# Kernel tuning notes

Hardware: AMD Instinct MI355X
Metric: run time of the kernel (lower is better)

The kernel has to match this reference:

```python
import jax, jax.numpy as jnp
import numpy as np

EPS = 1e-12

def l2norm(x):
    # matches torch F.normalize(dim=-1): x / max(||x||, eps)
    n = jnp.sqrt(jnp.sum(x * x, axis=-1, keepdims=True))
    return x / jnp.maximum(n, EPS)

def setup_inputs() -> dict:
    key = jax.random.key(0)
    ks = jax.random.split(key, 5)
    B, N, D, W = 128, 196, 768, 32
    image_features = jax.random.normal(ks[0], (B, D), jnp.float32)
    text_features = jax.random.normal(ks[1], (B, D), jnp.float32)
    image_token_features = jax.random.normal(ks[2], (B, N, D), jnp.float32)
    concept_text_features = jax.random.normal(ks[3], (B, W, D), jnp.float32)
    concept_counts = jax.random.randint(ks[4], (B,), 1, W + 1, dtype=jnp.int32)
    logit_scale = jnp.asarray(np.log(10.0), jnp.float32)   # SigLIP-style init
    logit_bias = jnp.asarray(-10.0, jnp.float32)
    return dict(image_features=image_features, text_features=text_features,
                image_token_features=image_token_features,
                concept_text_features=concept_text_features,
                concept_counts=concept_counts,
                logit_scale=logit_scale, logit_bias=logit_bias)

def _sigmoid_contrastive(logits):
    B = logits.shape[0]
    logits = jnp.clip(logits, -50.0, 50.0)
    z = 2.0 * jnp.eye(B, dtype=logits.dtype) - 1.0  # +1 diag, -1 off-diag
    return -jnp.mean(jax.nn.log_sigmoid(z * logits))

def reference(image_features, text_features, image_token_features,
              concept_text_features, concept_counts, logit_scale, logit_bias,
              alpha=0.5):
    t = jnp.exp(jnp.clip(logit_scale, -10.0, 10.0))

    # ---- IT-Align (SigLIP sigmoid contrastive on CLS features) ----
    img = l2norm(image_features)          # (B, D)
    txt = l2norm(text_features)           # (B, D)
    it_logits = t * (img @ txt.T) + logit_bias
    it_loss = _sigmoid_contrastive(it_logits)

    # ---- RC-Align (region-concept max-pool alignment, dense/masked) ----
    patches = l2norm(image_token_features)        # (B, N, D)
    concepts = l2norm(concept_text_features)      # (B, W, D)
    W = concepts.shape[1]
    # A[m, v, n, w] = cos(patch n of image m, concept w of sample v)
    A = jnp.einsum('mnd,vwd->mvnw', patches, concepts)
    max_per_concept = jnp.max(A, axis=2)          # (B, B, W) max over patches
    mask = (jnp.arange(W)[None, :] < concept_counts[:, None]).astype(patches.dtype)  # (B, W)
    counts = concept_counts.astype(patches.dtype)  # (B,)
    # S[m, v] = mean over valid concepts of sample v of max-pooled sims
    S = jnp.sum(max_per_concept * mask[None, :, :], axis=-1) / counts[None, :]
    rc_logits = t * S + logit_bias
    rc_loss = _sigmoid_contrastive(rc_logits)

    total = it_loss + alpha * rc_loss
    return total, it_loss, rc_loss
```

## Files before the change

kernel.cpp:

```cpp
#include <hip/hip_runtime.h>
#include <hip/hip_bf16.h>
#include <cstdint>

using i32x4 = __attribute__((ext_vector_type(4))) int;

#define BATCH   128
#define NPATCH  196
#define MTOT    25088
#define MT      98
#define DDIM    768
#define WCON    32
#define NCOLS   4096
#define BNC     128
#define NBN     32
#define NT      12
#define NBLK    3136

#define PB_PAT  0
#define NPAT2   (MTOT/2)
#define PB_CON  (NPAT2)
#define NCON2   (NCOLS/2)
#define PB_IMG  (PB_CON + NCON2)
#define PB_TXT  (PB_IMG + BATCH)
#define PB_MAX  (PB_TXT + BATCH)
#define PB_CIDX (PB_MAX + 64)
#define PB_N    (PB_CIDX + 1)

#define PI8_OFF   0ull
#define PI8_BYTES ((size_t)MTOT*DDIM)
#define CI8_OFF   (PI8_OFF + PI8_BYTES)
#define CI8_BYTES (4096ull*DDIM)
#define SP_OFF    (CI8_OFF + CI8_BYTES)
#define SP_BYTES  ((size_t)MTOT*4)
#define SC_OFF    (SP_OFF + SP_BYTES)
#define SC_BYTES  (4096ull*4)
#define IMGN_OFF  (SC_OFF + SC_BYTES)
#define F_BYTES   (128ull*768*4)
#define TXTN_OFF  (IMGN_OFF + F_BYTES)
#define MAX_OFF   (TXTN_OFF + F_BYTES)
#define MAX_BYTES (128ull*4096*4)
#define PART_OFF  (MAX_OFF + MAX_BYTES)
#define CIDX_OFF  (PART_OFF + 1024ull)
#define NCC_OFF   (CIDX_OFF + 4096ull*4)
#define WS_NEED   (NCC_OFF + 256ull)

__device__ __forceinline__ void async_cp16(void* lds_p, const void* g) {
  __builtin_amdgcn_global_load_lds(
      (const __attribute__((address_space(1))) unsigned int*)g,
      (__attribute__((address_space(3))) unsigned int*)lds_p, 16, 0, 0);
}

__device__ __forceinline__ float neg_log_sigmoid(float x) {
  return (x > 0.f) ? log1pf(expf(-x)) : (log1pf(expf(x)) - x);
}

__device__ __forceinline__ int encf(float f) {
  int i = __float_as_int(f);
  return i >= 0 ? i : (i ^ 0x7FFFFFFF);
}
__device__ __forceinline__ float decf(int e) {
  return __int_as_float(e >= 0 ? e : (e ^ 0x7FFFFFFF));
}

template<int VM>
__device__ __forceinline__ void vmwait() {
  asm volatile("s_waitcnt vmcnt(%0)" :: "n"(VM) : "memory");
}
__device__ __forceinline__ void blockbar() {
  asm volatile("" ::: "memory");
  __builtin_amdgcn_s_barrier();
  asm volatile("" ::: "memory");
}

__global__ void preproc_kernel(const float* __restrict__ tokp, char* __restrict__ outp,
                               float* __restrict__ srowp,
                               const float* __restrict__ tokc, char* __restrict__ outc,
                               float* __restrict__ srowc,
                               const float* __restrict__ imgf, float* __restrict__ imgn,
                               const float* __restrict__ txtf, float* __restrict__ txtn,
                               const int* __restrict__ counts,
                               int* __restrict__ Maxbuf,
                               int* __restrict__ cidx, int* __restrict__ ncc) {
  int bid = blockIdx.x;
  int t = threadIdx.x;

  if (bid >= PB_MAX) {
    if (bid < PB_CIDX) {
      int r = bid - PB_MAX;
      int4* dst = (int4*)(Maxbuf + (size_t)r * 8192);
      int4 pat = make_int4(0x80808080, 0x80808080, 0x80808080, 0x80808080);
      #pragma unroll
      for (int i = 0; i < 11; ++i) {
        int idx = t + i*192;
        if (idx < 2048) dst[idx] = pat;
      }
    } else {
      __shared__ int cls[128];
      __shared__ int stot;
      if (t < 128) cls[t] = counts[t];
      __syncthreads();
      if (t < 128) {
        int base = 0;
        for (int i = 0; i < t; ++i) base += cls[i];
        int cnt = cls[t];
        for (int k = 0; k < cnt; ++k) cidx[base + k] = t * 32 + k;
        if (t == 127) stot = base + cnt;
      }
      __syncthreads();
      if (t == 0) {
        int tot = stot;
        int totp = (tot + 127) & ~127;
        for (int j = tot; j < totp; ++j) cidx[j] = -1;
        ncc[0] = totp;
      }
    }
    return;
  }

  if (bid >= PB_IMG) {
    const float* in;
    float* fout;
    if (bid < PB_TXT) {
      int r = bid - PB_IMG;
      in = imgf + (size_t)r * DDIM; fout = imgn + (size_t)r * DDIM;
    } else {
      int r = bid - PB_TXT;
      in = txtf + (size_t)r * DDIM; fout = txtn + (size_t)r * DDIM;
    }
    __shared__ float sbs[3];
    float4 v = ((const float4*)in)[t];
    float ss = v.x*v.x + v.y*v.y + v.z*v.z + v.w*v.w;
    #pragma unroll
    for (int o = 32; o; o >>= 1) ss += __shfl_down(ss, o);
    if ((t & 63) == 0) sbs[t >> 6] = ss;
    __syncthreads();
    float tot = sbs[0] + sbs[1] + sbs[2];
    float scale = 1.0f / fmaxf(sqrtf(tot), 1e-12f);
    ((float4*)fout)[t] = make_float4(v.x*scale, v.y*scale, v.z*scale, v.w*scale);
    return;
  }

  const float *inA, *inB;
  char *qoutA, *qoutB;
  float *srowA, *srowB;
  bool validA = true, validB = true;
  if (bid < PB_CON) {
    int r = bid * 2;
    inA = tokp + (size_t)r * DDIM;       inB = inA + DDIM;
    qoutA = outp + (size_t)r * DDIM;     qoutB = qoutA + DDIM;
    srowA = srowp + r;                   srowB = srowA + 1;
  } else {
    int r = (bid - PB_CON) * 2;
    int cnt = counts[r >> 5];
    validA = (r & 31) < cnt;
    validB = ((r & 31) + 1) < cnt;
    if (!validA && !validB) return;
    inA = tokc + (size_t)r * DDIM;       inB = inA + DDIM;
    qoutA = outc + (size_t)r * DDIM;     qoutB = qoutA + DDIM;
    srowA = srowc + r;                   srowB = srowA + 1;
  }

  __shared__ float sA[3], aA[3], sB[3], aB[3];
  float4 vA = validA ? ((const float4*)inA)[t] : make_float4(0,0,0,0);
  float4 vB = validB ? ((const float4*)inB)[t] : make_float4(0,0,0,0);
  float ssA = vA.x*vA.x + vA.y*vA.y + vA.z*vA.z + vA.w*vA.w;
  float ssB = vB.x*vB.x + vB.y*vB.y + vB.z*vB.z + vB.w*vB.w;
  float amA = fmaxf(fmaxf(fabsf(vA.x), fabsf(vA.y)), fmaxf(fabsf(vA.z), fabsf(vA.w)));
  float amB = fmaxf(fmaxf(fabsf(vB.x), fabsf(vB.y)), fmaxf(fabsf(vB.z), fabsf(vB.w)));
  #pragma unroll
  for (int o = 32; o; o >>= 1) {
    ssA += __shfl_down(ssA, o);  amA = fmaxf(amA, __shfl_down(amA, o));
    ssB += __shfl_down(ssB, o);  amB = fmaxf(amB, __shfl_down(amB, o));
  }
  if ((t & 63) == 0) {
    sA[t >> 6] = ssA; aA[t >> 6] = amA;
    sB[t >> 6] = ssB; aB[t >> 6] = amB;
  }
  __syncthreads();
  float totA = sA[0] + sA[1] + sA[2];
  float totB = sB[0] + sB[1] + sB[2];
  float amxA = fmaxf(fmaxf(aA[0], aA[1]), fmaxf(aA[2], 1e-30f));
  float amxB = fmaxf(fmaxf(aB[0], aB[1]), fmaxf(aB[2], 1e-30f));

  if (validA) {
    float qs = 127.0f / amxA;
    int qx = (int)rintf(vA.x * qs), qy = (int)rintf(vA.y * qs);
    int qz = (int)rintf(vA.z * qs), qw = (int)rintf(vA.w * qs);
    ((uint*)qoutA)[t] = (uint)(qx & 0xff) | ((uint)(qy & 0xff) << 8) |
                        ((uint)(qz & 0xff) << 16) | ((uint)(qw & 0xff) << 24);
    if (t == 0) srowA[0] = amxA / (127.0f * fmaxf(sqrtf(totA), 1e-12f));
  }
  if (validB) {
    float qs = 127.0f / amxB;
    int qx = (int)rintf(vB.x * qs), qy = (int)rintf(vB.y * qs);
    int qz = (int)rintf(vB.z * qs), qw = (int)rintf(vB.w * qs);
    ((uint*)qoutB)[t] = (uint)(qx & 0xff) | ((uint)(qy & 0xff) << 8) |
                        ((uint)(qz & 0xff) << 16) | ((uint)(qw & 0xff) << 24);
    if (t == 0) srowB[0] = amxB / (127.0f * fmaxf(sqrtf(totB), 1e-12f));
  }
}

__global__ __launch_bounds__(256, 2)
void rc_gemm_max_kernel(const char* __restrict__ patches,
                        const char* __restrict__ concepts,
                        const float* __restrict__ sp,
                        const float* __restrict__ sc,
                        const int* __restrict__ cidx,
                        const int* __restrict__ ncc,
                        int* __restrict__ Max) {
  __shared__ __align__(16) char lds[3 * 24576];
  __shared__ float sp_lds[256];
  __shared__ float colmax[2][2][128];

  const int bid0 = blockIdx.x;
  const int lin = (bid0 & 7) * 392 + (bid0 >> 3);
  const int mt = lin >> 5;
  const int bn = lin & 31;
  const int bcol = bn * BNC;
  const int totp = __builtin_amdgcn_readfirstlane(ncc[0]);
  if (bcol >= totp) return;

  const int tid = threadIdx.x;
  const int lane = tid & 63;
  const int wid = tid >> 6;
  const int wm = wid >> 1;
  const int wn = wid & 1;
  const int brow = mt * 256;

  const char* Ab = patches + (size_t)brow * DDIM;

  sp_lds[tid] = sp[brow + tid];

  const int arow = wm*128 + (lane & 15);
  const int aslot = (lane >> 4) ^ (((lane & 15) >> 1) & 3);
  const int a_base = arow*64 + aslot*16;
  const int bcl = wn*64 + (lane & 15);
  const int b_base = 16384 + bcl*64 + aslot*16;
  const int r0 = tid >> 2;
  const int q0 = (tid & 3) ^ ((r0 >> 1) & 3);
  const int svoff = r0*DDIM + q0*16;

  const int cr0 = cidx[bcol + (tid >> 2)];
  const int cr1 = cidx[bcol + 64 + (tid >> 2)];
  const char* bp0 = concepts + (size_t)(cr0 < 0 ? 0 : cr0) * DDIM + q0*16;
  const char* bp1 = concepts + (size_t)(cr1 < 0 ? 0 : cr1) * DDIM + q0*16;

  i32x4 acc[8][4];
  #pragma unroll
  for (int i = 0; i < 8; ++i)
    #pragma unroll
    for (int j = 0; j < 4; ++j) { i32x4 z = {0,0,0,0}; acc[i][j] = z; }

  auto stage = [&](int t, int bufi) {
    char* dst = lds + bufi * 24576;
    const int kcol = t * 64;
    #pragma unroll
    for (int k2 = 0; k2 < 4; ++k2)
      async_cp16(dst + tid*16 + k2*4096, Ab + svoff + k2*(64*DDIM) + kcol);
    async_cp16(dst + 16384 + tid*16,        bp0 + kcol);
    async_cp16(dst + 16384 + tid*16 + 4096, bp1 + kcol);
  };

  auto compute = [&](int bufi) {
    const char* ab = lds + bufi * 24576;
    i32x4 a[8], b[4];
    #pragma unroll
    for (int i = 0; i < 8; ++i) a[i] = *(const i32x4*)(ab + a_base + i*1024);
    #pragma unroll
    for (int j = 0; j < 4; ++j) b[j] = *(const i32x4*)(ab + b_base + j*1024);
    __builtin_amdgcn_s_setprio(1);
    #pragma unroll
    for (int i = 0; i < 8; ++i)
      #pragma unroll
      for (int j = 0; j < 4; ++j)
        acc[i][j] = __builtin_amdgcn_mfma_i32_16x16x64_i8(a[i], b[j], acc[i][j], 0, 0, 0);
    __builtin_amdgcn_s_setprio(0);
  };

#define TILE(T, VMN, DOSTAGE)                                                 \
  {                                                                           \
    if (DOSTAGE) stage((T) + 2, ((T) + 2) % 3);                               \
    vmwait<VMN>();                                                            \
    blockbar();                                                               \
    compute((T) % 3);                                                         \
    blockbar();                                                               \
  }

  stage(0, 0);
  stage(1, 1);
  TILE(0, 12, 1)  TILE(1, 12, 1)  TILE(2, 12, 1)  TILE(3, 12, 1)
  TILE(4, 12, 1)  TILE(5, 12, 1)  TILE(6, 12, 1)  TILE(7, 12, 1)
  TILE(8, 12, 1)  TILE(9, 12, 1)  TILE(10, 6, 0)  TILE(11, 0, 0)
#undef TILE

  float cmax[4][2];
  #pragma unroll
  for (int j = 0; j < 4; ++j) { cmax[j][0] = -3e38f; cmax[j][1] = -3e38f; }
  float scv[4];
  #pragma unroll
  for (int j = 0; j < 4; ++j) {
    int oc = cidx[bcol + wn*64 + j*16 + (lane & 15)];
    scv[j] = sc[oc < 0 ? 0 : oc];
  }
  const int img0w = (brow + wm*128) / NPATCH;
  #pragma unroll
  for (int i = 0; i < 8; ++i) {
    #pragma unroll
    for (int e = 0; e < 4; ++e) {
      int rl = wm*128 + i*16 + (lane >> 4)*4 + e;
      float spv = sp_lds[rl];
      int seg = ((brow + rl) / NPATCH) - img0w;
      #pragma unroll
      for (int j = 0; j < 4; ++j) {
        float v = (float)acc[i][j][e] * spv * scv[j];
        cmax[j][0] = (seg == 0) ? fmaxf(cmax[j][0], v) : cmax[j][0];
        cmax[j][1] = (seg == 1) ? fmaxf(cmax[j][1], v) : cmax[j][1];
      }
    }
  }
  #pragma unroll
  for (int j = 0; j < 4; ++j) {
    #pragma unroll
    for (int s = 0; s < 2; ++s) {
      float v = cmax[j][s];
      v = fmaxf(v, __shfl_xor(v, 16));
      v = fmaxf(v, __shfl_xor(v, 32));
      cmax[j][s] = v;
    }
  }
  if (lane < 16) {
    #pragma unroll
    for (int j = 0; j < 4; ++j) {
      colmax[wm][0][wn*64 + j*16 + lane] = cmax[j][0];
      colmax[wm][1][wn*64 + j*16 + lane] = cmax[j][1];
    }
  }
  __syncthreads();
  {
    int w = tid >> 7;
    int col = tid & 127;
    int oc = cidx[bcol + col];
    if (oc >= 0) {
      int i0 = (brow + w*128) / NPATCH;
      int i1 = (brow + w*128 + 127) / NPATCH;
      atomicMax(&Max[(size_t)i0 * NCOLS + oc], encf(colmax[w][0][col]));
      if (i1 != i0) atomicMax(&Max[(size_t)i1 * NCOLS + oc], encf(colmax[w][1][col]));
    }
  }
}

__global__ void loss_kernel(const float* __restrict__ imgn, const float* __restrict__ txtn,
                            const int* __restrict__ Max, const int* __restrict__ counts,
                            const float* __restrict__ sc, const float* __restrict__ bi,
                            float* __restrict__ part) {
  int bid = blockIdx.x;
  int c = threadIdx.x;
  float t = expf(fminf(fmaxf(sc[0], -10.f), 10.f));
  float val;
  int m;
  if (bid < BATCH) {
    m = bid;
    __shared__ __align__(16) float arow[DDIM];
    for (int k = c; k < DDIM; k += 128) arow[k] = imgn[(size_t)m * DDIM + k];
    __syncthreads();
    const float4* br = (const float4*)(txtn + (size_t)c * DDIM);
    const float4* ar = (const float4*)arow;
    float dot = 0.f;
    #pragma unroll 8
    for (int k = 0; k < DDIM/4; ++k) {
      float4 x = ar[k], y = br[k];
      dot += x.x*y.x + x.y*y.y + x.z*y.z + x.w*y.w;
    }
    float logit = fminf(fmaxf(t*dot + bi[0], -50.f), 50.f);
    val = neg_log_sigmoid((c == m) ? logit : -logit);
  } else {
    m = bid - BATCH;
    const int* row = Max + (size_t)m * NCOLS + (size_t)c * WCON;
    int cnt = counts[c];
    float s = 0.f;
    for (int w = 0; w < cnt; ++w) s += decf(row[w]);
    float S = s / (float)cnt;
    float logit = fminf(fmaxf(t*S + bi[0], -50.f), 50.f);
    val = neg_log_sigmoid((c == m) ? logit : -logit);
  }
  __shared__ float sb[2];
  #pragma unroll
  for (int o = 32; o; o >>= 1) val += __shfl_down(val, o);
  if ((c & 63) == 0) sb[c >> 6] = val;
  __syncthreads();
  if (c == 0) part[bid] = sb[0] + sb[1];
}

__global__ void finalize_kernel(const float* __restrict__ part, float* __restrict__ out) {
  int t = threadIdx.x;
  float v = part[t];
  __shared__ float sb[4];
  #pragma unroll
  for (int o = 32; o; o >>= 1) v += __shfl_down(v, o);
  if ((t & 63) == 0) sb[t >> 6] = v;
  __syncthreads();
  if (t == 0) {
    float it = (sb[0] + sb[1]) * (1.f / 16384.f);
    float rc = (sb[2] + sb[3]) * (1.f / 16384.f);
    out[0] = it + 0.5f * rc;
    out[1] = it;
    out[2] = rc;
  }
}


extern "C" void kernel_launch(void* const* d_in, const int* in_sizes, int n_in,
                              void* d_out, int out_size, void* d_ws, size_t ws_size,
                              hipStream_t stream) {
  const float* image_features        = (const float*)d_in[0];
  const float* text_features         = (const float*)d_in[1];
  const float* image_token_features  = (const float*)d_in[2];
  const float* concept_text_features = (const float*)d_in[3];
  const int*   concept_counts        = (const int*)d_in[4];
  const float* logit_scale           = (const float*)d_in[5];
  const float* logit_bias            = (const float*)d_in[6];
  float* out = (float*)d_out;

  if (ws_size < WS_NEED) {
    hipMemsetAsync(d_out, 0, (size_t)out_size * sizeof(float), stream);
    return;
  }

  char* ws = (char*)d_ws;
  char*  patches_i8  = ws + PI8_OFF;
  char*  concepts_i8 = ws + CI8_OFF;
  float* sp          = (float*)(ws + SP_OFF);
  float* scq         = (float*)(ws + SC_OFF);
  float* imgn        = (float*)(ws + IMGN_OFF);
  float* txtn        = (float*)(ws + TXTN_OFF);
  int*   Maxbuf      = (int*)(ws + MAX_OFF);
  float* part        = (float*)(ws + PART_OFF);
  int*   cidx        = (int*)(ws + CIDX_OFF);
  int*   ncc         = (int*)(ws + NCC_OFF);

  preproc_kernel<<<PB_N, 192, 0, stream>>>(
      image_token_features, patches_i8, sp,
      concept_text_features, concepts_i8, scq,
      image_features, imgn, text_features, txtn,
      concept_counts, Maxbuf, cidx, ncc);

  rc_gemm_max_kernel<<<NBLK, 256, 0, stream>>>(patches_i8, concepts_i8, sp, scq,
                                               cidx, ncc, Maxbuf);

  loss_kernel<<<2*BATCH, 128, 0, stream>>>(imgn, txtn, Maxbuf, concept_counts,
                                           logit_scale, logit_bias, part);
  finalize_kernel<<<1, 256, 0, stream>>>(part, out);
}
```

Baseline: 105.6 us.

## Split tail-wave GEMM tiles into half-height blocks to balance the last wave

The GEMM launch now enumerates only the active tiles, using the concept count read from the device, instead of launching the full grid and early-exiting. Tiles beyond the last multiple of 512 are split into two 128-row half tiles via a templated body, so the final partial wave has more, smaller blocks. This targets tail-wave underutilisation on the 256-CU device. In exchange the grid size is fixed at 3648 and the half tiles do more concept loads per output.

Result: slower. 158.6 us (+50.2%).

```diff
diff --git a/kernel.cpp b/kernel.cpp
--- a/kernel.cpp
+++ b/kernel.cpp
@@ -12,9 +12,7 @@
 #define WCON    32
 #define NCOLS   4096
 #define BNC     128
-#define NBN     32
-#define NT      12
-#define NBLK    3136
+#define NBLKG   3648
 
 #define PB_PAT  0
 #define NPAT2   (MTOT/2)
@@ -200,6 +198,144 @@
   }
 }
 
+template<int MR>
+__device__ __forceinline__ void gemm_body(
+    const char* __restrict__ Ab,
+    const char* __restrict__ concepts,
+    const float* __restrict__ sp,
+    const float* __restrict__ sc,
+    const int* __restrict__ cidx,
+    int brow, int bcol, int* __restrict__ Max,
+    char* lds, float* sp_lds, float* colmax, int tid) {
+  constexpr int ROWS = MR * 32;
+  constexpr int ACP  = ROWS / 64;
+  constexpr int L    = ACP + 2;
+
+  const int lane = tid & 63;
+  const int wid = tid >> 6;
+  const int wm = wid >> 1;
+  const int wn = wid & 1;
+
+  if (tid < ROWS) sp_lds[tid] = sp[brow + tid];
+
+  const int arow = wm*(MR*16) + (lane & 15);
+  const int aslot = (lane >> 4) ^ (((lane & 15) >> 1) & 3);
+  const int a_base = arow*64 + aslot*16;
+  const int bcl = wn*64 + (lane & 15);
+  const int b_base = 16384 + bcl*64 + aslot*16;
+  const int r0 = tid >> 2;
+  const int q0 = (tid & 3) ^ ((r0 >> 1) & 3);
+  const int svoff = r0*DDIM + q0*16;
+
+  const int cr0 = cidx[bcol + (tid >> 2)];
+  const int cr1 = cidx[bcol + 64 + (tid >> 2)];
+  const char* bp0 = concepts + (size_t)(cr0 < 0 ? 0 : cr0) * DDIM + q0*16;
+  const char* bp1 = concepts + (size_t)(cr1 < 0 ? 0 : cr1) * DDIM + q0*16;
+
+  i32x4 acc[MR][4];
+  #pragma unroll
+  for (int i = 0; i < MR; ++i)
+    #pragma unroll
+    for (int j = 0; j < 4; ++j) { i32x4 z = {0,0,0,0}; acc[i][j] = z; }
+
+  auto stage = [&](int t, int bufi) {
+    char* dst = lds + bufi * 24576;
+    const int kcol = t * 64;
+    #pragma unroll
+    for (int k2 = 0; k2 < ACP; ++k2)
+      async_cp16(dst + tid*16 + k2*4096, Ab + svoff + k2*(64*DDIM) + kcol);
+    async_cp16(dst + 16384 + tid*16,        bp0 + kcol);
+    async_cp16(dst + 16384 + tid*16 + 4096, bp1 + kcol);
+  };
+
+  auto compute = [&](int bufi) {
+    const char* ab = lds + bufi * 24576;
+    i32x4 a[MR], b[4];
+    #pragma unroll
+    for (int i = 0; i < MR; ++i) a[i] = *(const i32x4*)(ab + a_base + i*1024);
+    #pragma unroll
+    for (int j = 0; j < 4; ++j) b[j] = *(const i32x4*)(ab + b_base + j*1024);
+    __builtin_amdgcn_s_setprio(1);
+    #pragma unroll
+    for (int i = 0; i < MR; ++i)
+      #pragma unroll
+      for (int j = 0; j < 4; ++j)
+        acc[i][j] = __builtin_amdgcn_mfma_i32_16x16x64_i8(a[i], b[j], acc[i][j], 0, 0, 0);
+    __builtin_amdgcn_s_setprio(0);
+  };
+
+#define TILE(T, VMN, DOSTAGE)                                                 \
+  {                                                                           \
+    if (DOSTAGE) stage((T) + 2, ((T) + 2) % 3);                               \
+    vmwait<VMN>();                                                            \
+    blockbar();                                                               \
+    compute((T) % 3);                                                         \
+    blockbar();                                                               \
+  }
+
+  stage(0, 0);
+  stage(1, 1);
+  TILE(0, 2*L, 1)  TILE(1, 2*L, 1)  TILE(2, 2*L, 1)  TILE(3, 2*L, 1)
+  TILE(4, 2*L, 1)  TILE(5, 2*L, 1)  TILE(6, 2*L, 1)  TILE(7, 2*L, 1)
+  TILE(8, 2*L, 1)  TILE(9, 2*L, 1)  TILE(10, L, 0)   TILE(11, 0, 0)
+#undef TILE
+
+  float cmax[4][2];
+  #pragma unroll
+  for (int j = 0; j < 4; ++j) { cmax[j][0] = -3e38f; cmax[j][1] = -3e38f; }
+  float scv[4];
+  #pragma unroll
+  for (int j = 0; j < 4; ++j) {
+    int oc = cidx[bcol + wn*64 + j*16 + (lane & 15)];
+    scv[j] = sc[oc < 0 ? 0 : oc];
+  }
+  const int img0w = (brow + wm*(MR*16)) / NPATCH;
+  #pragma unroll
+  for (int i = 0; i < MR; ++i) {
+    #pragma unroll
+    for (int e = 0; e < 4; ++e) {
+      int rl = wm*(MR*16) + i*16 + (lane >> 4)*4 + e;
+      float spv = sp_lds[rl];
+      int seg = ((brow + rl) / NPATCH) - img0w;
+      #pragma unroll
+      for (int j = 0; j < 4; ++j) {
+        float v = (float)acc[i][j][e] * spv * scv[j];
+        cmax[j][0] = (seg == 0) ? fmaxf(cmax[j][0], v) : cmax[j][0];
+        cmax[j][1] = (seg == 1) ? fmaxf(cmax[j][1], v) : cmax[j][1];
+      }
+    }
+  }
+  #pragma unroll
+  for (int j = 0; j < 4; ++j) {
+    #pragma unroll
+    for (int s = 0; s < 2; ++s) {
+      float v = cmax[j][s];
+      v = fmaxf(v, __shfl_xor(v, 16));
+      v = fmaxf(v, __shfl_xor(v, 32));
+      cmax[j][s] = v;
+    }
+  }
+  if (lane < 16) {
+    #pragma unroll
+    for (int j = 0; j < 4; ++j) {
+      colmax[(wm*2 + 0)*128 + wn*64 + j*16 + lane] = cmax[j][0];
+      colmax[(wm*2 + 1)*128 + wn*64 + j*16 + lane] = cmax[j][1];
+    }
+  }
+  __syncthreads();
+  {
+    int w = tid >> 7;
+    int col = tid & 127;
+    int oc = cidx[bcol + col];
+    if (oc >= 0) {
+      int i0 = (brow + w*(MR*16)) / NPATCH;
+      int i1 = (brow + w*(MR*16) + MR*16 - 1) / NPATCH;
+      atomicMax(&Max[(size_t)i0 * NCOLS + oc], encf(colmax[(w*2 + 0)*128 + col]));
+      if (i1 != i0) atomicMax(&Max[(size_t)i1 * NCOLS + oc], encf(colmax[(w*2 + 1)*128 + col]));
+    }
+  }
+}
+
 __global__ __launch_bounds__(256, 2)
 void rc_gemm_max_kernel(const char* __restrict__ patches,
                         const char* __restrict__ concepts,
@@ -210,142 +346,40 @@
                         int* __restrict__ Max) {
   __shared__ __align__(16) char lds[3 * 24576];
   __shared__ float sp_lds[256];
-  __shared__ float colmax[2][2][128];
+  __shared__ float colmax[512];
+
+  const int totp = __builtin_amdgcn_readfirstlane(ncc[0]);
+  const int nbn = totp >> 7;
+  const int nact = MT * nbn;
+  const int nfull = nact & ~511;
+  const int nsplit = nact - nfull;
 
   const int bid0 = blockIdx.x;
-  const int lin = (bid0 & 7) * 392 + (bid0 >> 3);
-  const int mt = lin >> 5;
-  const int bn = lin & 31;
+  const int lin = (bid0 & 7) * (NBLKG/8) + (bid0 >> 3);
+
+  int c, mhalf = -1;
+  if (lin < nfull) {
+    c = lin;
+  } else if (lin < nfull + 2*nsplit) {
+    int s = lin - nfull;
+    c = nfull + (s >> 1);
+    mhalf = s & 1;
+  } else {
+    return;
+  }
+  const int mt = c / nbn;
+  const int bn = c - mt * nbn;
   const int bcol = bn * BNC;
-  const int totp = __builtin_amdgcn_readfirstlane(ncc[0]);
-  if (bcol >= totp) return;
-
   const int tid = threadIdx.x;
-  const int lane = tid & 63;
-  const int wid = tid >> 6;
-  const int wm = wid >> 1;
-  const int wn = wid & 1;
-  const int brow = mt * 256;
-
-  const char* Ab = patches + (size_t)brow * DDIM;
-
-  sp_lds[tid] = sp[brow + tid];
-
-  const int arow = wm*128 + (lane & 15);
-  const int aslot = (lane >> 4) ^ (((lane & 15) >> 1) & 3);
-  const int a_base = arow*64 + aslot*16;
-  const int bcl = wn*64 + (lane & 15);
-  const int b_base = 16384 + bcl*64 + aslot*16;
-  const int r0 = tid >> 2;
-  const int q0 = (tid & 3) ^ ((r0 >> 1) & 3);
-  const int svoff = r0*DDIM + q0*16;
-
-  const int cr0 = cidx[bcol + (tid >> 2)];
-  const int cr1 = cidx[bcol + 64 + (tid >> 2)];
-  const char* bp0 = concepts + (size_t)(cr0 < 0 ? 0 : cr0) * DDIM + q0*16;
-  const char* bp1 = concepts + (size_t)(cr1 < 0 ? 0 : cr1) * DDIM + q0*16;
-
-  i32x4 acc[8][4];
-  #pragma unroll
-  for (int i = 0; i < 8; ++i)
-    #pragma unroll
-    for (int j = 0; j < 4; ++j) { i32x4 z = {0,0,0,0}; acc[i][j] = z; }
-
-  auto stage = [&](int t, int bufi) {
-    char* dst = lds + bufi * 24576;
-    const int kcol = t * 64;
-    #pragma unroll
-    for (int k2 = 0; k2 < 4; ++k2)
-      async_cp16(dst + tid*16 + k2*4096, Ab + svoff + k2*(64*DDIM) + kcol);
-    async_cp16(dst + 16384 + tid*16,        bp0 + kcol);
-    async_cp16(dst + 16384 + tid*16 + 4096, bp1 + kcol);
-  };
-
-  auto compute = [&](int bufi) {
-    const char* ab = lds + bufi * 24576;
-    i32x4 a[8], b[4];
-    #pragma unroll
-    for (int i = 0; i < 8; ++i) a[i] = *(const i32x4*)(ab + a_base + i*1024);
-    #pragma unroll
-    for (int j = 0; j < 4; ++j) b[j] = *(const i32x4*)(ab + b_base + j*1024);
-    __builtin_amdgcn_s_setprio(1);
-    #pragma unroll
-    for (int i = 0; i < 8; ++i)
-      #pragma unroll
-      for (int j = 0; j < 4; ++j)
-        acc[i][j] = __builtin_amdgcn_mfma_i32_16x16x64_i8(a[i], b[j], acc[i][j], 0, 0, 0);
-    __builtin_amdgcn_s_setprio(0);
-  };
-
-#define TILE(T, VMN, DOSTAGE)                                                 \
-  {                                                                           \
-    if (DOSTAGE) stage((T) + 2, ((T) + 2) % 3);                               \
-    vmwait<VMN>();                                                            \
-    blockbar();                                                               \
-    compute((T) % 3);                                                         \
-    blockbar();                                                               \
-  }
-
-  stage(0, 0);
-  stage(1, 1);
-  TILE(0, 12, 1)  TILE(1, 12, 1)  TILE(2, 12, 1)  TILE(3, 12, 1)
-  TILE(4, 12, 1)  TILE(5, 12, 1)  TILE(6, 12, 1)  TILE(7, 12, 1)
-  TILE(8, 12, 1)  TILE(9, 12, 1)  TILE(10, 6, 0)  TILE(11, 0, 0)
-#undef TILE
-
-  float cmax[4][2];
-  #pragma unroll
-  for (int j = 0; j < 4; ++j) { cmax[j][0] = -3e38f; cmax[j][1] = -3e38f; }
-  float scv[4];
-  #pragma unroll
-  for (int j = 0; j < 4; ++j) {
-    int oc = cidx[bcol + wn*64 + j*16 + (lane & 15)];
-    scv[j] = sc[oc < 0 ? 0 : oc];
-  }
-  const int img0w = (brow + wm*128) / NPATCH;
-  #pragma unroll
-  for (int i = 0; i < 8; ++i) {
-    #pragma unroll
-    for (int e = 0; e < 4; ++e) {
-      int rl = wm*128 + i*16 + (lane >> 4)*4 + e;
-      float spv = sp_lds[rl];
-      int seg = ((brow + rl) / NPATCH) - img0w;
-      #pragma unroll
-      for (int j = 0; j < 4; ++j) {
-        float v = (float)acc[i][j][e] * spv * scv[j];
-        cmax[j][0] = (seg == 0) ? fmaxf(cmax[j][0], v) : cmax[j][0];
-        cmax[j][1] = (seg == 1) ? fmaxf(cmax[j][1], v) : cmax[j][1];
-      }
-    }
-  }
-  #pragma unroll
-  for (int j = 0; j < 4; ++j) {
-    #pragma unroll
-    for (int s = 0; s < 2; ++s) {
-      float v = cmax[j][s];
-      v = fmaxf(v, __shfl_xor(v, 16));
-      v = fmaxf(v, __shfl_xor(v, 32));
-      cmax[j][s] = v;
-    }
-  }
-  if (lane < 16) {
-    #pragma unroll
-    for (int j = 0; j < 4; ++j) {
-      colmax[wm][0][wn*64 + j*16 + lane] = cmax[j][0];
-      colmax[wm][1][wn*64 + j*16 + lane] = cmax[j][1];
-    }
-  }
-  __syncthreads();
-  {
-    int w = tid >> 7;
-    int col = tid & 127;
-    int oc = cidx[bcol + col];
-    if (oc >= 0) {
-      int i0 = (brow + w*128) / NPATCH;
-      int i1 = (brow + w*128 + 127) / NPATCH;
-      atomicMax(&Max[(size_t)i0 * NCOLS + oc], encf(colmax[w][0][col]));
-      if (i1 != i0) atomicMax(&Max[(size_t)i1 * NCOLS + oc], encf(colmax[w][1][col]));
-    }
+
+  if (mhalf < 0) {
+    int brow = mt * 256;
+    gemm_body<8>(patches + (size_t)brow * DDIM, concepts, sp, sc, cidx,
+                 brow, bcol, Max, lds, sp_lds, colmax, tid);
+  } else {
+    int brow = mt * 256 + mhalf * 128;
+    gemm_body<4>(patches + (size_t)brow * DDIM, concepts, sp, sc, cidx,
+                 brow, bcol, Max, lds, sp_lds, colmax, tid);
   }
 }
 
@@ -444,8 +478,8 @@
       image_features, imgn, text_features, txtn,
       concept_counts, Maxbuf, cidx, ncc);
 
-  rc_gemm_max_kernel<<<NBLK, 256, 0, stream>>>(patches_i8, concepts_i8, sp, scq,
-                                               cidx, ncc, Maxbuf);
+  rc_gemm_max_kernel<<<NBLKG, 256, 0, stream>>>(patches_i8, concepts_i8, sp, scq,
+                                                cidx, ncc, Maxbuf);
 
   loss_kernel<<<2*BATCH, 128, 0, stream>>>(imgn, txtn, Maxbuf, concept_counts,
                                            logit_scale, logit_bias, part);
```
